# Optimization experiments

Hardware: AMD Instinct MI355X
Metric: run time of the kernel (lower is better)

The kernel has to match this reference:

```python
import jax, jax.numpy as jnp
import numpy as np


def setup_inputs() -> dict:
    key = jax.random.key(0)
    k1, k2 = jax.random.split(key)
    x = jax.random.normal(k1, (32, 512, 512, 1), dtype=jnp.float32)
    se = jnp.ones((3, 3), dtype=jnp.float32)
    rank = jax.random.normal(k2, (9,), dtype=jnp.float32)
    return {"x": x, "se": se, "rank": rank}


def _extract_patches_3x3_same(x):
    # x: [B, H, W, 1] -> [B, H, W, 9], zero-padded SAME, row-major window order
    B, H, W, C = x.shape
    xp = jnp.pad(x, ((0, 0), (1, 1), (1, 1), (0, 0)))
    shifts = [xp[:, dy:dy + H, dx:dx + W, 0] for dy in range(3) for dx in range(3)]
    return jnp.stack(shifts, axis=-1)  # [B, H, W, 9]


def reference(x, se, rank):
    # Faithful to Morph2D.call: patches * se, sort ascending over the 9-window,
    # softmax(rank)-weighted sum -> soft rank-order filter.
    patches = _extract_patches_3x3_same(x)              # [B,H,W,9]
    weighted = patches * se.reshape(9)                  # elementwise by SE
    sorted_p = jnp.sort(weighted, axis=-1)              # ascending over window
    w = jax.nn.softmax(rank)                            # [9]
    out = jnp.sum(sorted_p * w, axis=-1)                # [B,H,W]
    return out.reshape(x.shape)                         # [B,H,W,1]
```

## Files before the change

kernel.cpp:

```cpp
#include <hip/hip_runtime.h>


#define BB 32
#define HH 512
#define WW 512

__global__ void prep_weights(const float* __restrict__ rank, float* __restrict__ w) {
    if (threadIdx.x == 0 && blockIdx.x == 0) {
        float r[9];
        float m = -3.4e38f;
        #pragma unroll
        for (int i = 0; i < 9; ++i) { r[i] = rank[i]; m = fmaxf(m, r[i]); }
        float s = 0.f;
        #pragma unroll
        for (int i = 0; i < 9; ++i) { r[i] = expf(r[i] - m); s += r[i]; }
        float inv = 1.0f / s;
        #pragma unroll
        for (int i = 0; i < 9; ++i) w[i] = r[i] * inv;
    }
}

#define CSWAP(a,b) { float lo_ = fminf(v[a], v[b]); float hi_ = fmaxf(v[a], v[b]); v[a] = lo_; v[b] = hi_; }

__global__ __launch_bounds__(256) void morph2d_kernel(
    const float* __restrict__ x, const float* __restrict__ se9,
    const float* __restrict__ w9, float* __restrict__ out)
{
    int g  = blockIdx.x * blockDim.x + threadIdx.x;
    int gx = g & 127;
    int y  = (g >> 7) & 511;
    int b  = g >> 16;
    int x4 = gx << 2;

    float se[9], w[9];
    #pragma unroll
    for (int i = 0; i < 9; ++i) { se[i] = se9[i]; w[i] = w9[i]; }

    float rowv[3][6];
    #pragma unroll
    for (int dy = 0; dy < 3; ++dy) {
        int ry = y + dy - 1;
        if (ry < 0 || ry >= HH) {
            #pragma unroll
            for (int i = 0; i < 6; ++i) rowv[dy][i] = 0.f;
        } else {
            const float* r = x + ((size_t)b * HH + ry) * WW;
            float4 c = *(const float4*)(r + x4);
            rowv[dy][1] = c.x; rowv[dy][2] = c.y; rowv[dy][3] = c.z; rowv[dy][4] = c.w;
            rowv[dy][0] = (x4 == 0)        ? 0.f : r[x4 - 1];
            rowv[dy][5] = (x4 + 4 >= WW)   ? 0.f : r[x4 + 4];
        }
    }

    float4 res;
    float* resp = &res.x;
    #pragma unroll
    for (int j = 0; j < 4; ++j) {
        float v[9];
        #pragma unroll
        for (int dy = 0; dy < 3; ++dy) {
            v[dy*3+0] = rowv[dy][j]   * se[dy*3+0];
            v[dy*3+1] = rowv[dy][j+1] * se[dy*3+1];
            v[dy*3+2] = rowv[dy][j+2] * se[dy*3+2];
        }
        CSWAP(0,3) CSWAP(1,7) CSWAP(2,5) CSWAP(4,8)
        CSWAP(0,7) CSWAP(2,4) CSWAP(3,8) CSWAP(5,6)
        CSWAP(0,2) CSWAP(1,3) CSWAP(4,5) CSWAP(7,8)
        CSWAP(1,4) CSWAP(3,6) CSWAP(5,7)
        CSWAP(0,1) CSWAP(2,4) CSWAP(3,5) CSWAP(6,8)
        CSWAP(2,3) CSWAP(4,5) CSWAP(6,7)
        CSWAP(1,2) CSWAP(3,4) CSWAP(5,6)

        float acc = 0.f;
        #pragma unroll
        for (int i = 0; i < 9; ++i) acc = fmaf(v[i], w[i], acc);
        resp[j] = acc;
    }

    *(float4*)(out + (((size_t)b * HH + y) * WW + x4)) = res;
}

extern "C" void kernel_launch(void* const* d_in, const int* in_sizes, int n_in,
                              void* d_out, int out_size, void* d_ws, size_t ws_size,
                              hipStream_t stream) {
    const float* x    = (const float*)d_in[0];
    const float* se   = (const float*)d_in[1];
    const float* rank = (const float*)d_in[2];
    float* w9  = (float*)d_ws;
    float* out = (float*)d_out;

    prep_weights<<<1, 64, 0, stream>>>(rank, w9);

    const int total_groups = BB * HH * (WW / 4);
    morph2d_kernel<<<total_groups / 256, 256, 0, stream>>>(x, se, w9, out);
}
```

Before: 97.55 us.

## Fuse softmax into main kernel, compute two rows per thread, swizzle blocks

Removes the separate single-thread softmax launch and recomputes the softmax weights per thread with fast exp inside the filter kernel. Each thread now produces two output rows from four loaded input rows, cutting redundant row loads from three per output row to two. Block indices are remapped across 8 groups, likely to spread work across XCDs. Halo rows are clamped and masked instead of branched. The cost is more registers per thread and half as many threads.

```diff
diff --git a/kernel.cpp b/kernel.cpp
--- a/kernel.cpp
+++ b/kernel.cpp
@@ -5,79 +5,82 @@
 #define HH 512
 #define WW 512
 
-__global__ void prep_weights(const float* __restrict__ rank, float* __restrict__ w) {
-    if (threadIdx.x == 0 && blockIdx.x == 0) {
-        float r[9];
-        float m = -3.4e38f;
+#define CSWAP(a,b) { float lo_ = fminf(v[a], v[b]); float hi_ = fmaxf(v[a], v[b]); v[a] = lo_; v[b] = hi_; }
+
+__global__ __launch_bounds__(256) void morph2d_kernel(
+    const float* __restrict__ x, const float* __restrict__ se9,
+    const float* __restrict__ rank, float* __restrict__ out)
+{
+    int nper = gridDim.x >> 3;
+    int lb   = (blockIdx.x & 7) * nper + (blockIdx.x >> 3);
+    int g    = lb * 256 + threadIdx.x;
+
+    int gx = g & 127;
+    int yg = (g >> 7) & 255;
+    int b  = g >> 15;
+    int x4 = gx << 2;
+    int y0 = yg << 1;
+
+    float se[9], w[9];
+    {
+        float r[9]; float m = -3.4e38f;
         #pragma unroll
         for (int i = 0; i < 9; ++i) { r[i] = rank[i]; m = fmaxf(m, r[i]); }
         float s = 0.f;
         #pragma unroll
-        for (int i = 0; i < 9; ++i) { r[i] = expf(r[i] - m); s += r[i]; }
+        for (int i = 0; i < 9; ++i) { r[i] = __expf(r[i] - m); s += r[i]; }
         float inv = 1.0f / s;
         #pragma unroll
-        for (int i = 0; i < 9; ++i) w[i] = r[i] * inv;
-    }
-}
-
-#define CSWAP(a,b) { float lo_ = fminf(v[a], v[b]); float hi_ = fmaxf(v[a], v[b]); v[a] = lo_; v[b] = hi_; }
-
-__global__ __launch_bounds__(256) void morph2d_kernel(
-    const float* __restrict__ x, const float* __restrict__ se9,
-    const float* __restrict__ w9, float* __restrict__ out)
-{
-    int g  = blockIdx.x * blockDim.x + threadIdx.x;
-    int gx = g & 127;
-    int y  = (g >> 7) & 511;
-    int b  = g >> 16;
-    int x4 = gx << 2;
-
-    float se[9], w[9];
-    #pragma unroll
-    for (int i = 0; i < 9; ++i) { se[i] = se9[i]; w[i] = w9[i]; }
-
-    float rowv[3][6];
-    #pragma unroll
-    for (int dy = 0; dy < 3; ++dy) {
-        int ry = y + dy - 1;
-        if (ry < 0 || ry >= HH) {
-            #pragma unroll
-            for (int i = 0; i < 6; ++i) rowv[dy][i] = 0.f;
-        } else {
-            const float* r = x + ((size_t)b * HH + ry) * WW;
-            float4 c = *(const float4*)(r + x4);
-            rowv[dy][1] = c.x; rowv[dy][2] = c.y; rowv[dy][3] = c.z; rowv[dy][4] = c.w;
-            rowv[dy][0] = (x4 == 0)        ? 0.f : r[x4 - 1];
-            rowv[dy][5] = (x4 + 4 >= WW)   ? 0.f : r[x4 + 4];
-        }
+        for (int i = 0; i < 9; ++i) { w[i] = r[i] * inv; se[i] = se9[i]; }
     }
 
-    float4 res;
-    float* resp = &res.x;
+    const float* img = x + (size_t)b * (HH * WW);
+    float rv[4][6];
     #pragma unroll
-    for (int j = 0; j < 4; ++j) {
-        float v[9];
-        #pragma unroll
-        for (int dy = 0; dy < 3; ++dy) {
-            v[dy*3+0] = rowv[dy][j]   * se[dy*3+0];
-            v[dy*3+1] = rowv[dy][j+1] * se[dy*3+1];
-            v[dy*3+2] = rowv[dy][j+2] * se[dy*3+2];
-        }
-        CSWAP(0,3) CSWAP(1,7) CSWAP(2,5) CSWAP(4,8)
-        CSWAP(0,7) CSWAP(2,4) CSWAP(3,8) CSWAP(5,6)
-        CSWAP(0,2) CSWAP(1,3) CSWAP(4,5) CSWAP(7,8)
-        CSWAP(1,4) CSWAP(3,6) CSWAP(5,7)
-        CSWAP(0,1) CSWAP(2,4) CSWAP(3,5) CSWAP(6,8)
-        CSWAP(2,3) CSWAP(4,5) CSWAP(6,7)
-        CSWAP(1,2) CSWAP(3,4) CSWAP(5,6)
-
-        float acc = 0.f;
-        #pragma unroll
-        for (int i = 0; i < 9; ++i) acc = fmaf(v[i], w[i], acc);
-        resp[j] = acc;
+    for (int r = 0; r < 4; ++r) {
+        int ry  = y0 - 1 + r;
+        int ryc = min(max(ry, 0), HH - 1);
+        const float* row = img + ryc * WW;
+        float4 c  = *(const float4*)(row + x4);
+        float  lf = row[max(x4 - 1, 0)];
+        float  rt = row[min(x4 + 4, WW - 1)];
+        float  m  = (ry >= 0 && ry < HH) ? 1.0f : 0.0f;
+        rv[r][0] = ((x4 == 0)       ? 0.f : lf) * m;
+        rv[r][1] = c.x * m;
+        rv[r][2] = c.y * m;
+        rv[r][3] = c.z * m;
+        rv[r][4] = c.w * m;
+        rv[r][5] = ((x4 + 4 >= WW)  ? 0.f : rt) * m;
     }
 
-    *(float4*)(out + (((size_t)b * HH + y) * WW + x4)) = res;
+    #pragma unroll
+    for (int r = 0; r < 2; ++r) {
+        float4 res;
+        float* resp = &res.x;
+        #pragma unroll
+        for (int j = 0; j < 4; ++j) {
+            float v[9];
+            #pragma unroll
+            for (int dy = 0; dy < 3; ++dy) {
+                v[dy*3+0] = rv[r+dy][j]   * se[dy*3+0];
+                v[dy*3+1] = rv[r+dy][j+1] * se[dy*3+1];
+                v[dy*3+2] = rv[r+dy][j+2] * se[dy*3+2];
+            }
+            CSWAP(0,3) CSWAP(1,7) CSWAP(2,5) CSWAP(4,8)
+            CSWAP(0,7) CSWAP(2,4) CSWAP(3,8) CSWAP(5,6)
+            CSWAP(0,2) CSWAP(1,3) CSWAP(4,5) CSWAP(7,8)
+            CSWAP(1,4) CSWAP(3,6) CSWAP(5,7)
+            CSWAP(0,1) CSWAP(2,4) CSWAP(3,5) CSWAP(6,8)
+            CSWAP(2,3) CSWAP(4,5) CSWAP(6,7)
+            CSWAP(1,2) CSWAP(3,4) CSWAP(5,6)
+
+            float acc = 0.f;
+            #pragma unroll
+            for (int i = 0; i < 9; ++i) acc = fmaf(v[i], w[i], acc);
+            resp[j] = acc;
+        }
+        *(float4*)(out + (((size_t)b * HH + (y0 + r)) * WW + x4)) = res;
+    }
 }
 
 extern "C" void kernel_launch(void* const* d_in, const int* in_sizes, int n_in,
@@ -86,11 +89,8 @@
     const float* x    = (const float*)d_in[0];
     const float* se   = (const float*)d_in[1];
     const float* rank = (const float*)d_in[2];
-    float* w9  = (float*)d_ws;
     float* out = (float*)d_out;
 
-    prep_weights<<<1, 64, 0, stream>>>(rank, w9);
-
-    const int total_groups = BB * HH * (WW / 4);
-    morph2d_kernel<<<total_groups / 256, 256, 0, stream>>>(x, se, w9, out);
+    const int total_threads = BB * (HH / 2) * (WW / 4);
+    morph2d_kernel<<<total_threads / 256, 256, 0, stream>>>(x, se, rank, out);
 }
```

After: 101.1 us. 3.7% more time.
